# Optimization experiments

Measured on AMD Instinct MI355X. Metric: run time of the kernel, lower is better.

The kernel has to match this reference:

```python
import jax, jax.numpy as jnp
import numpy as np

B, S, D, H = 4, 1024, 1024, 16
HD = D // H  # 64
EPS = 1e-5

def _ln(x, g, b):
    m = jnp.mean(x, axis=-1, keepdims=True)
    v = jnp.mean(jnp.square(x - m), axis=-1, keepdims=True)
    return (x - m) * jax.lax.rsqrt(v + EPS) * g + b

def setup_inputs() -> dict:
    key = jax.random.key(0)
    ks = jax.random.split(key, 16)
    std = 0.02
    return {
        "query_tokens": jax.random.normal(ks[0], (B, S, D), jnp.float32),
        "keyvalue_tokens": jax.random.normal(ks[1], (B, S, D), jnp.float32),
        "ln_q_g": jnp.ones((D,), jnp.float32),
        "ln_q_b": jnp.zeros((D,), jnp.float32),
        "ln_kv_g": jnp.ones((D,), jnp.float32),
        "ln_kv_b": jnp.zeros((D,), jnp.float32),
        "Wq": jax.random.normal(ks[2], (2 * D, D), jnp.float32) * std,
        "Wk": jax.random.normal(ks[3], (2 * D, D), jnp.float32) * std,
        "Wv": jax.random.normal(ks[4], (2 * D, D), jnp.float32) * std,
        "Wo": jax.random.normal(ks[5], (D, 2 * D), jnp.float32) * std,
        "lambda_q1": jax.random.normal(ks[6], (HD,), jnp.float32) * 0.1,
        "lambda_k1": jax.random.normal(ks[7], (HD,), jnp.float32) * 0.1,
        "lambda_q2": jax.random.normal(ks[8], (HD,), jnp.float32) * 0.1,
        "lambda_k2": jax.random.normal(ks[9], (HD,), jnp.float32) * 0.1,
        "hn_g": jnp.ones((2 * HD,), jnp.float32),
        "hn_b": jnp.zeros((2 * HD,), jnp.float32),
        "lambda_init": jnp.float32(0.8),
        "disable_second_term": 0,
    }

def reference(query_tokens, keyvalue_tokens, ln_q_g, ln_q_b, ln_kv_g, ln_kv_b,
              Wq, Wk, Wv, Wo, lambda_q1, lambda_k1, lambda_q2, lambda_k2,
              hn_g, hn_b, lambda_init, disable_second_term):
    scale = 1.0 / np.sqrt(HD)
    q_ln = _ln(query_tokens, ln_q_g, ln_q_b)
    kv_ln = _ln(keyvalue_tokens, ln_kv_g, ln_kv_b)
    # projections: torch Linear => x @ W.T ; reshape to [B, H, S, 2*HD]
    def proj(x, W):
        y = jnp.einsum('bsd,ed->bse', x, W)
        return y.reshape(B, S, H, 2 * HD).transpose(0, 2, 1, 3)
    q = proj(q_ln, Wq)
    k = proj(kv_ln, Wk)
    v = proj(kv_ln, Wv)
    q1, q2 = q[..., :HD], q[..., HD:]
    k1, k2 = k[..., :HD], k[..., HD:]
    scores1 = jnp.einsum('bhsd,bhtd->bhst', q1, k1) * scale
    scores2 = jnp.einsum('bhsd,bhtd->bhst', q2, k2) * scale
    attn1 = jax.nn.softmax(scores1, axis=-1)
    attn2 = jax.nn.softmax(scores2, axis=-1)
    if disable_second_term:
        lam = jnp.zeros((), query_tokens.dtype)
    else:
        lam = (jnp.exp(jnp.dot(lambda_q1, lambda_k1))
               - jnp.exp(jnp.dot(lambda_q2, lambda_k2)) + lambda_init)
    out = jnp.einsum('bhst,bhtd->bhsd', attn1 - lam * attn2, v)  # [B,H,S,2HD]
    out = _ln(out, hn_g, hn_b) * (1.0 - lambda_init)
    out = out.transpose(0, 2, 1, 3).reshape(B, S, 2 * D)
    out = jnp.einsum('bse,de->bsd', out, Wo)
    return query_tokens + out
```

## Files before the change

kernel.cpp:

```cpp
#include <hip/hip_runtime.h>
#include <stdint.h>

#define B_  4
#define S_  1024
#define D_  1024
#define H_  16
#define HD_ 64
#define E_  2048
#define C2_ 128

typedef __attribute__((ext_vector_type(8))) short          bf16x8;
typedef __attribute__((ext_vector_type(8))) unsigned short u16x8;
typedef __attribute__((ext_vector_type(4))) unsigned short u16x4;
typedef __attribute__((ext_vector_type(4))) float          f32x4;

#define QSCALE 0.18033688f

__device__ __forceinline__ unsigned short f2bf(float f) {
  union { float f; unsigned int u; } v; v.f = f;
  unsigned int r = v.u + 0x7fffu + ((v.u >> 16) & 1u);
  return (unsigned short)(r >> 16);
}

__device__ __forceinline__ unsigned int cvtpk_bf16(float lo, float hi) {
  unsigned int r;
  asm("v_cvt_pk_bf16_f32 %0, %1, %2" : "=v"(r) : "v"(lo), "v"(hi));
  return r;
}

__device__ __forceinline__ float red16_sum(float x) {
  x += __int_as_float(__builtin_amdgcn_mov_dpp(__float_as_int(x), 0xB1, 0xF, 0xF, false));
  x += __int_as_float(__builtin_amdgcn_mov_dpp(__float_as_int(x), 0x4E, 0xF, 0xF, false));
  x += __int_as_float(__builtin_amdgcn_mov_dpp(__float_as_int(x), 0x141, 0xF, 0xF, false));
  x += __int_as_float(__builtin_amdgcn_mov_dpp(__float_as_int(x), 0x140, 0xF, 0xF, false));
  return x;
}

typedef const __attribute__((address_space(1))) unsigned int* gas1_t;
typedef __attribute__((address_space(3))) unsigned int* las3_t;
__device__ __forceinline__ void gload16(const void* g, void* s) {
  __builtin_amdgcn_global_load_lds((gas1_t)g, (las3_t)s, 16, 0, 0);
}

__global__ __launch_bounds__(256) void ln2_cast_k(const float* __restrict__ xq,
                                                  const float* __restrict__ xkv,
                                                  const float* __restrict__ gq,
                                                  const float* __restrict__ bq,
                                                  const float* __restrict__ gkv,
                                                  const float* __restrict__ bkv,
                                                  unsigned short* __restrict__ oq,
                                                  unsigned short* __restrict__ okv) {
  int sel = blockIdx.y;
  const float* x = sel ? xkv : xq;
  const float* g = sel ? gkv : gq;
  const float* bb = sel ? bkv : bq;
  unsigned short* out = sel ? okv : oq;
  int row = blockIdx.x;
  int tid = threadIdx.x;
  const float* xr = x + (size_t)row * D_;
  float4 xv = *(const float4*)(xr + tid * 4);
  float s  = xv.x + xv.y + xv.z + xv.w;
  float sq = xv.x * xv.x + xv.y * xv.y + xv.z * xv.z + xv.w * xv.w;
#pragma unroll
  for (int m = 32; m; m >>= 1) { s += __shfl_xor(s, m, 64); sq += __shfl_xor(sq, m, 64); }
  __shared__ float ps[4], pq[4];
  int w = tid >> 6, l = tid & 63;
  if (l == 0) { ps[w] = s; pq[w] = sq; }
  __syncthreads();
  s  = ps[0] + ps[1] + ps[2] + ps[3];
  sq = pq[0] + pq[1] + pq[2] + pq[3];
  float mean = s * (1.f / D_);
  float var  = sq * (1.f / D_) - mean * mean;
  float rstd = rsqrtf(var + 1e-5f);
  float4 gv = *(const float4*)(g + tid * 4);
  float4 bv = *(const float4*)(bb + tid * 4);
  u16x4 o;
  o.x = f2bf((xv.x - mean) * rstd * gv.x + bv.x);
  o.y = f2bf((xv.y - mean) * rstd * gv.y + bv.y);
  o.z = f2bf((xv.z - mean) * rstd * gv.z + bv.z);
  o.w = f2bf((xv.w - mean) * rstd * gv.w + bv.w);
  *(u16x4*)(out + (size_t)row * D_ + tid * 4) = o;
}

__global__ __launch_bounds__(256) void cast4_k(const float* __restrict__ i0, const float* __restrict__ i1,
                                               const float* __restrict__ i2, const float* __restrict__ i3,
                                               unsigned short* __restrict__ o0, unsigned short* __restrict__ o1,
                                               unsigned short* __restrict__ o2, unsigned short* __restrict__ o3,
                                               int n4) {
  int sel = blockIdx.y;
  const float* in = (sel == 0) ? i0 : (sel == 1) ? i1 : (sel == 2) ? i2 : i3;
  unsigned short* out = (sel == 0) ? o0 : (sel == 1) ? o1 : (sel == 2) ? o2 : o3;
  int i = blockIdx.x * 256 + threadIdx.x;
  if (i < n4) {
    float4 v = *(const float4*)(in + (size_t)i * 4);
    u16x4 o; o.x = f2bf(v.x); o.y = f2bf(v.y); o.z = f2bf(v.z); o.w = f2bf(v.w);
    *(u16x4*)(out + (size_t)i * 4) = o;
  }
}

__global__ __launch_bounds__(256) void gemm_proj_k(
    const unsigned short* __restrict__ qln, const unsigned short* __restrict__ kvln,
    const unsigned short* __restrict__ Wq,  const unsigned short* __restrict__ Wk,
    const unsigned short* __restrict__ Wv,
    unsigned short* __restrict__ qb, unsigned short* __restrict__ kb,
    unsigned short* __restrict__ vtb) {
  const int K = D_;
  int which = blockIdx.z;
  const unsigned short* A = (which == 0) ? qln : kvln;
  const unsigned short* W = (which == 0) ? Wq : (which == 1 ? Wk : Wv);
  unsigned short* O = (which == 0) ? qb : (which == 1 ? kb : vtb);
  int m0 = blockIdx.y * 128, n0 = blockIdx.x * 128;
  __shared__ __align__(16) char psm[128 * 272];
  char* lsA = psm;
  char* lsB = psm + 16384;
  int tid = threadIdx.x, l = tid & 63, w = tid >> 6;
  int wm = (w >> 1) * 64, wn = (w & 1) * 64;
  f32x4 acc[4][4] = {};
  for (int kt = 0; kt < K; kt += 64) {
    __syncthreads();
#pragma unroll
    for (int i = 0; i < 4; i++) {
      int rbase = (i * 4 + w) * 8;
      int row = rbase + (l >> 3), c8 = l & 7;
      int sc = (c8 ^ (row & 7)) * 8;
      gload16(A + (size_t)(m0 + row) * K + kt + sc, lsA + rbase * 128);
      gload16(W + (size_t)(n0 + row) * K + kt + sc, lsB + rbase * 128);
    }
    __syncthreads();
#pragma unroll
    for (int kk = 0; kk < 2; kk++) {
      bf16x8 af[4], bfr[4];
      int koff = kk * 64 + (l >> 4) * 16;
#pragma unroll
      for (int mf = 0; mf < 4; mf++) {
        int row = wm + mf * 16 + (l & 15);
        af[mf] = *(const bf16x8*)(lsA + row * 128 + (koff ^ ((row & 7) << 4)));
      }
#pragma unroll
      for (int nf = 0; nf < 4; nf++) {
        int row = wn + nf * 16 + (l & 15);
        bfr[nf] = *(const bf16x8*)(lsB + row * 128 + (koff ^ ((row & 7) << 4)));
      }
#pragma unroll
      for (int mf = 0; mf < 4; mf++)
#pragma unroll
        for (int nf = 0; nf < 4; nf++)
          acc[mf][nf] = __builtin_amdgcn_mfma_f32_16x16x32_bf16(af[mf], bfr[nf], acc[mf][nf], 0, 0, 0);
    }
  }
  if (which < 2) {
    float sc = (which == 0) ? QSCALE : 1.0f;
#pragma unroll
    for (int mf = 0; mf < 4; mf++)
#pragma unroll
      for (int nf = 0; nf < 4; nf++)
#pragma unroll
        for (int r = 0; r < 4; r++) {
          int gm = m0 + wm + mf * 16 + (l >> 4) * 4 + r;
          int gn = n0 + wn + nf * 16 + (l & 15);
          int b = gm >> 10, s = gm & 1023;
          int h = gn >> 7,  c = gn & 127;
          O[((size_t)((b * H_ + h) * S_ + s)) * C2_ + c] = f2bf(acc[mf][nf][r] * sc);
        }
  } else {
    __syncthreads();
#pragma unroll
    for (int mf = 0; mf < 4; mf++)
#pragma unroll
      for (int nf = 0; nf < 4; nf++) {
        int crow = wn + nf * 16 + (l & 15);
        int sloc = wm + mf * 16 + (l >> 4) * 4;
        u16x4 pk4;
        pk4.x = f2bf(acc[mf][nf][0]); pk4.y = f2bf(acc[mf][nf][1]);
        pk4.z = f2bf(acc[mf][nf][2]); pk4.w = f2bf(acc[mf][nf][3]);
        *(u16x4*)(psm + (size_t)crow * 272 + sloc * 2) = pk4;
      }
    __syncthreads();
    int b = m0 >> 10, sbase = m0 & 1023;
#pragma unroll
    for (int i = 0; i < 8; i++) {
      int u2 = i * 256 + tid;
      int row = u2 >> 4, c16 = u2 & 15;
      u16x8 vv = *(const u16x8*)(psm + (size_t)row * 272 + c16 * 16);
      int gn = n0 + row, h = gn >> 7, cfeat = gn & 127;
      *(u16x8*)(O + ((size_t)((b * H_ + h) * C2_ + cfeat)) * S_ + sbase + c16 * 8) = vv;
    }
  }
}

__global__ __launch_bounds__(256) void gemm_out_k(
    const unsigned short* __restrict__ A, const unsigned short* __restrict__ W,
    const float* __restrict__ resid, float* __restrict__ out) {
  const int K = E_;
  int m0 = blockIdx.y * 128, n0 = blockIdx.x * 128;
  __shared__ __align__(16) char psm2[32768];
  char* lsA = psm2;
  char* lsB = psm2 + 16384;
  int tid = threadIdx.x, l = tid & 63, w = tid >> 6;
  int wm = (w >> 1) * 64, wn = (w & 1) * 64;
  f32x4 acc[4][4] = {};
  for (int kt = 0; kt < K; kt += 64) {
    __syncthreads();
#pragma unroll
    for (int i = 0; i < 4; i++) {
      int rbase = (i * 4 + w) * 8;
      int row = rbase + (l >> 3), c8 = l & 7;
      int sc = (c8 ^ (row & 7)) * 8;
      gload16(A + (size_t)(m0 + row) * K + kt + sc, lsA + rbase * 128);
      gload16(W + (size_t)(n0 + row) * K + kt + sc, lsB + rbase * 128);
    }
    __syncthreads();
#pragma unroll
    for (int kk = 0; kk < 2; kk++) {
      bf16x8 af[4], bfr[4];
      int koff = kk * 64 + (l >> 4) * 16;
#pragma unroll
      for (int mf = 0; mf < 4; mf++) {
        int row = wm + mf * 16 + (l & 15);
        af[mf] = *(const bf16x8*)(lsA + row * 128 + (koff ^ ((row & 7) << 4)));
      }
#pragma unroll
      for (int nf = 0; nf < 4; nf++) {
        int row = wn + nf * 16 + (l & 15);
        bfr[nf] = *(const bf16x8*)(lsB + row * 128 + (koff ^ ((row & 7) << 4)));
      }
#pragma unroll
      for (int mf = 0; mf < 4; mf++)
#pragma unroll
        for (int nf = 0; nf < 4; nf++)
          acc[mf][nf] = __builtin_amdgcn_mfma_f32_16x16x32_bf16(af[mf], bfr[nf], acc[mf][nf], 0, 0, 0);
    }
  }
#pragma unroll
  for (int mf = 0; mf < 4; mf++)
#pragma unroll
    for (int nf = 0; nf < 4; nf++)
#pragma unroll
      for (int r = 0; r < 4; r++) {
        int gm = m0 + wm + mf * 16 + (l >> 4) * 4 + r;
        int gn = n0 + wn + nf * 16 + (l & 15);
        size_t idx = (size_t)gm * D_ + gn;
        out[idx] = acc[mf][nf][r] + resid[idx];
      }
}

__global__ __launch_bounds__(256) void attn_k(
    const unsigned short* __restrict__ q, const unsigned short* __restrict__ k,
    const unsigned short* __restrict__ vt,
    const float* __restrict__ lq1, const float* __restrict__ lk1,
    const float* __restrict__ lq2, const float* __restrict__ lk2,
    const float* __restrict__ hng, const float* __restrict__ hnb,
    const float* __restrict__ lambda_init, const int* __restrict__ dis2,
    unsigned short* __restrict__ out) {
  int bh = blockIdx.x;
  int qt = blockIdx.y;
  int tid = threadIdx.x, ln = tid & 63, w = tid >> 6;
  int g = ln >> 4, c = ln & 15;
  __shared__ unsigned short lsK[64 * 128];
  __shared__ unsigned short lsVt[128 * 64];
  __shared__ float s_lam, s_osc;

  if (tid < 64) {
    float a = lq1[ln] * lk1[ln];
    float cc = lq2[ln] * lk2[ln];
#pragma unroll
    for (int m = 32; m; m >>= 1) { a += __shfl_xor(a, m, 64); cc += __shfl_xor(cc, m, 64); }
    if (ln == 0) {
      float li = lambda_init[0];
      float lam = __expf(a) - __expf(cc) + li;
      if (dis2[0] != 0) lam = 0.f;
      s_lam = lam;
      s_osc = 1.f - li;
    }
  }

  const unsigned short* kbh = k + (size_t)bh * S_ * C2_;
  const unsigned short* vbh = vt + (size_t)bh * C2_ * S_;

  int qrow = qt * 64 + w * 16 + c;
  const unsigned short* qrp = q + ((size_t)bh * S_ + qrow) * C2_;
  bf16x8 qf[2][2];
#pragma unroll
  for (int t = 0; t < 2; t++)
#pragma unroll
    for (int kk = 0; kk < 2; kk++)
      qf[t][kk] = *(const bf16x8*)(qrp + t * 64 + kk * 32 + g * 8);

  f32x4 lones[2] = {};
  f32x4 o[2][8] = {};
  bf16x8 onesf;
#pragma unroll
  for (int j = 0; j < 8; j++) onesf[j] = (short)0x3F80;

#define STAGE_KV(t0s)                                                                 \
  {                                                                                   \
    const unsigned short* kbase = kbh + (size_t)(t0s) * C2_;                          \
    _Pragma("unroll")                                                                 \
    for (int i = 0; i < 4; i++) {                                                     \
      int rb = w * 16 + i * 4;                                                        \
      int row = rb + (ln >> 4), c16 = ln & 15;                                        \
      gload16(kbase + row * C2_ + ((c16 ^ (row & 7)) * 8),                            \
              (char*)&lsK[0] + rb * 256);                                             \
    }                                                                                 \
    const unsigned short* vbase = vbh + (t0s);                                        \
    _Pragma("unroll")                                                                 \
    for (int i = 0; i < 4; i++) {                                                     \
      int rb = w * 32 + i * 8;                                                        \
      int row = rb + (ln >> 3), c8 = ln & 7;                                          \
      gload16(vbase + (size_t)row * S_ + ((c8 ^ (row & 7)) * 8),                      \
              (char*)&lsVt[0] + rb * 128);                                            \
    }                                                                                 \
  }

  for (int t0 = 0; t0 < S_; t0 += 64) {
    STAGE_KV(t0);
    __syncthreads();

    unsigned int paw[2][2][4];

#pragma unroll
    for (int term = 0; term < 2; term++) {
      f32x4 sf[4] = {};
      __builtin_amdgcn_s_setprio(1);
#pragma unroll
      for (int kk = 0; kk < 2; kk++) {
#pragma unroll
        for (int nf = 0; nf < 4; nf++) {
          int kfrow = nf * 16 + c;
          bf16x8 kf = *(const bf16x8*)((char*)&lsK[0] + kfrow * 256 +
                        ((term * 128 + kk * 64 + g * 16) ^ ((kfrow & 7) << 4)));
          sf[nf] = __builtin_amdgcn_mfma_f32_16x16x32_bf16(kf, qf[term][kk], sf[nf], 0, 0, 0);
        }
      }
      __builtin_amdgcn_s_setprio(0);
#pragma unroll
      for (int nf = 0; nf < 4; nf++)
#pragma unroll
        for (int r = 0; r < 4; r++)
          sf[nf][r] = exp2f(sf[nf][r]);
#pragma unroll
      for (int kk = 0; kk < 2; kk++) {
        unsigned int X0 = cvtpk_bf16(sf[2 * kk][0], sf[2 * kk][1]);
        unsigned int X1 = cvtpk_bf16(sf[2 * kk][2], sf[2 * kk][3]);
        unsigned int Y0 = cvtpk_bf16(sf[2 * kk + 1][0], sf[2 * kk + 1][1]);
        unsigned int Y1 = cvtpk_bf16(sf[2 * kk + 1][2], sf[2 * kk + 1][3]);
        asm("v_permlane32_swap_b32 %0, %1" : "+v"(X0), "+v"(Y0));
        asm("v_permlane32_swap_b32 %0, %1" : "+v"(X1), "+v"(Y1));
        asm("v_permlane16_swap_b32 %0, %1" : "+v"(X0), "+v"(Y0));
        asm("v_permlane16_swap_b32 %0, %1" : "+v"(X1), "+v"(Y1));
        paw[term][kk][0] = X0; paw[term][kk][1] = X1;
        paw[term][kk][2] = Y0; paw[term][kk][3] = Y1;
      }
    }

#pragma unroll
    for (int kk = 0; kk < 2; kk++) {
      union { unsigned int u[4]; bf16x8 v; } pa0, pa1;
#pragma unroll
      for (int j = 0; j < 4; j++) { pa0.u[j] = paw[0][kk][j]; pa1.u[j] = paw[1][kk][j]; }
      __builtin_amdgcn_s_setprio(1);
      lones[0] = __builtin_amdgcn_mfma_f32_16x16x32_bf16(pa0.v, onesf, lones[0], 0, 0, 0);
      lones[1] = __builtin_amdgcn_mfma_f32_16x16x32_bf16(pa1.v, onesf, lones[1], 0, 0, 0);
#pragma unroll
      for (int nf2 = 0; nf2 < 8; nf2++) {
        int vrow = nf2 * 16 + c;
        bf16x8 vf = *(const bf16x8*)((char*)&lsVt[0] + vrow * 128 +
                      ((kk * 64 + g * 16) ^ ((vrow & 7) << 4)));
        o[0][nf2] = __builtin_amdgcn_mfma_f32_16x16x32_bf16(pa0.v, vf, o[0][nf2], 0, 0, 0);
        o[1][nf2] = __builtin_amdgcn_mfma_f32_16x16x32_bf16(pa1.v, vf, o[1][nf2], 0, 0, 0);
      }
      __builtin_amdgcn_s_setprio(0);
    }
    __syncthreads();
  }

  float lam = s_lam, osc = s_osc;
  int b = bh >> 4, h = bh & 15;
#pragma unroll
  for (int r = 0; r < 4; r++) {
    float inv1 = 1.f / lones[0][r];
    float inv2 = lam / lones[1][r];
    float vals[8];
    float sum = 0.f, sq = 0.f;
#pragma unroll
    for (int nf2 = 0; nf2 < 8; nf2++) {
      float vv = o[0][nf2][r] * inv1 - o[1][nf2][r] * inv2;
      vals[nf2] = vv;
      sum += vv; sq += vv * vv;
    }
    sum = red16_sum(sum);
    sq  = red16_sum(sq);
    float mean = sum * (1.f / 128.f);
    float var  = sq * (1.f / 128.f) - mean * mean;
    float rstd = rsqrtf(var + 1e-5f);
    int srow = qt * 64 + w * 16 + g * 4 + r;
    unsigned short* orow = out + ((size_t)(b * S_ + srow)) * E_ + h * C2_;
#pragma unroll
    for (int nf2 = 0; nf2 < 8; nf2++) {
      int feat = nf2 * 16 + c;
      float y = (vals[nf2] - mean) * rstd * hng[feat] + hnb[feat];
      orow[feat] = f2bf(y * osc);
    }
  }
}

extern "C" void kernel_launch(void* const* d_in, const int* in_sizes, int n_in,
                              void* d_out, int out_size, void* d_ws, size_t ws_size,
                              hipStream_t stream) {
  const float* qtok = (const float*)d_in[0];
  const float* kvtok = (const float*)d_in[1];
  const float* lnqg = (const float*)d_in[2];
  const float* lnqb = (const float*)d_in[3];
  const float* lnkg = (const float*)d_in[4];
  const float* lnkb = (const float*)d_in[5];
  const float* Wq = (const float*)d_in[6];
  const float* Wk = (const float*)d_in[7];
  const float* Wv = (const float*)d_in[8];
  const float* Wo = (const float*)d_in[9];
  const float* lq1 = (const float*)d_in[10];
  const float* lk1 = (const float*)d_in[11];
  const float* lq2 = (const float*)d_in[12];
  const float* lk2 = (const float*)d_in[13];
  const float* hng = (const float*)d_in[14];
  const float* hnb = (const float*)d_in[15];
  const float* lami = (const float*)d_in[16];
  const int*   dis2 = (const int*)d_in[17];
  float* outp = (float*)d_out;

  char* ws = (char*)d_ws;
  const size_t MB = 1024 * 1024;
  unsigned short* qln    = (unsigned short*)(ws + 0);
  unsigned short* kvln   = (unsigned short*)(ws + 8 * MB);
  unsigned short* attn_o = (unsigned short*)(ws + 0);
  unsigned short* Wqb = (unsigned short*)(ws + 16 * MB);
  unsigned short* Wkb = (unsigned short*)(ws + 20 * MB);
  unsigned short* Wvb = (unsigned short*)(ws + 24 * MB);
  unsigned short* Wob = (unsigned short*)(ws + 28 * MB);
  unsigned short* qb  = (unsigned short*)(ws + 32 * MB);
  unsigned short* kb  = (unsigned short*)(ws + 48 * MB);
  unsigned short* vtb = (unsigned short*)(ws + 64 * MB);

  ln2_cast_k<<<dim3(4096, 2), dim3(256), 0, stream>>>(qtok, kvtok, lnqg, lnqb, lnkg, lnkb, qln, kvln);
  cast4_k<<<dim3(2048, 4), dim3(256), 0, stream>>>(Wq, Wk, Wv, Wo, Wqb, Wkb, Wvb, Wob, 512 * 1024);
  gemm_proj_k<<<dim3(16, 32, 3), dim3(256), 0, stream>>>(qln, kvln, Wqb, Wkb, Wvb, qb, kb, vtb);
  attn_k<<<dim3(64, 16), dim3(256), 0, stream>>>(qb, kb, vtb, lq1, lk1, lq2, lk2,
                                                 hng, hnb, lami, dis2, attn_o);
  gemm_out_k<<<dim3(8, 32), dim3(256), 0, stream>>>(attn_o, Wob, qtok, outp);
}
```

Before: 206.3 us.

## Double-buffer K/V LDS tiles with 32-key chunks to overlap loads with MFMA

Splits the key loop into 32-key chunks and adds two LDS buffers for K and Vt, so the next chunk is prefetched while the current one is computed. The Vt LDS layout and swizzle change to fit the narrower tile. The goal is to hide global-to-LDS latency behind the matrix work. In exchange there are twice as many iterations and barriers, and each barrier covers less MFMA work.

```diff
diff --git a/kernel.cpp b/kernel.cpp
--- a/kernel.cpp
+++ b/kernel.cpp
@@ -256,8 +256,8 @@
   int qt = blockIdx.y;
   int tid = threadIdx.x, ln = tid & 63, w = tid >> 6;
   int g = ln >> 4, c = ln & 15;
-  __shared__ unsigned short lsK[64 * 128];
-  __shared__ unsigned short lsVt[128 * 64];
+  __shared__ unsigned short lsK[2][32 * 128];
+  __shared__ unsigned short lsVt[2][128 * 32];
   __shared__ float s_lam, s_osc;
 
   if (tid < 64) {
@@ -292,80 +292,81 @@
 #pragma unroll
   for (int j = 0; j < 8; j++) onesf[j] = (short)0x3F80;
 
-#define STAGE_KV(t0s)                                                                 \
+#define STAGE_KV(buf, t0s)                                                            \
   {                                                                                   \
     const unsigned short* kbase = kbh + (size_t)(t0s) * C2_;                          \
     _Pragma("unroll")                                                                 \
-    for (int i = 0; i < 4; i++) {                                                     \
-      int rb = w * 16 + i * 4;                                                        \
+    for (int i = 0; i < 2; i++) {                                                     \
+      int rb = w * 8 + i * 4;                                                         \
       int row = rb + (ln >> 4), c16 = ln & 15;                                        \
       gload16(kbase + row * C2_ + ((c16 ^ (row & 7)) * 8),                            \
-              (char*)&lsK[0] + rb * 256);                                             \
+              (char*)&lsK[buf][0] + rb * 256);                                        \
     }                                                                                 \
     const unsigned short* vbase = vbh + (t0s);                                        \
     _Pragma("unroll")                                                                 \
-    for (int i = 0; i < 4; i++) {                                                     \
-      int rb = w * 32 + i * 8;                                                        \
-      int row = rb + (ln >> 3), c8 = ln & 7;                                          \
-      gload16(vbase + (size_t)row * S_ + ((c8 ^ (row & 7)) * 8),                      \
-              (char*)&lsVt[0] + rb * 128);                                            \
+    for (int i = 0; i < 2; i++) {                                                     \
+      int rb = w * 32 + i * 16;                                                       \
+      int row = rb + (ln >> 2), c4 = ln & 3;                                          \
+      gload16(vbase + (size_t)row * S_ + ((c4 ^ ((row >> 1) & 3)) * 8),               \
+              (char*)&lsVt[buf][0] + rb * 64);                                        \
     }                                                                                 \
   }
 
-  for (int t0 = 0; t0 < S_; t0 += 64) {
-    STAGE_KV(t0);
-    __syncthreads();
-
-    unsigned int paw[2][2][4];
+  STAGE_KV(0, 0);
+  __syncthreads();
+
+  for (int it = 0; it < S_ / 32; ++it) {
+    int cur = it & 1;
+    if (it + 1 < S_ / 32) STAGE_KV(cur ^ 1, (it + 1) * 32);
+
+    unsigned int paw[2][4];
 
 #pragma unroll
     for (int term = 0; term < 2; term++) {
-      f32x4 sf[4] = {};
+      f32x4 sf[2] = {};
       __builtin_amdgcn_s_setprio(1);
 #pragma unroll
       for (int kk = 0; kk < 2; kk++) {
 #pragma unroll
-        for (int nf = 0; nf < 4; nf++) {
+        for (int nf = 0; nf < 2; nf++) {
           int kfrow = nf * 16 + c;
-          bf16x8 kf = *(const bf16x8*)((char*)&lsK[0] + kfrow * 256 +
+          bf16x8 kf = *(const bf16x8*)((char*)&lsK[cur][0] + kfrow * 256 +
                         ((term * 128 + kk * 64 + g * 16) ^ ((kfrow & 7) << 4)));
           sf[nf] = __builtin_amdgcn_mfma_f32_16x16x32_bf16(kf, qf[term][kk], sf[nf], 0, 0, 0);
         }
       }
       __builtin_amdgcn_s_setprio(0);
 #pragma unroll
-      for (int nf = 0; nf < 4; nf++)
+      for (int nf = 0; nf < 2; nf++)
 #pragma unroll
         for (int r = 0; r < 4; r++)
           sf[nf][r] = exp2f(sf[nf][r]);
-#pragma unroll
-      for (int kk = 0; kk < 2; kk++) {
-        unsigned int X0 = cvtpk_bf16(sf[2 * kk][0], sf[2 * kk][1]);
-        unsigned int X1 = cvtpk_bf16(sf[2 * kk][2], sf[2 * kk][3]);
-        unsigned int Y0 = cvtpk_bf16(sf[2 * kk + 1][0], sf[2 * kk + 1][1]);
-        unsigned int Y1 = cvtpk_bf16(sf[2 * kk + 1][2], sf[2 * kk + 1][3]);
+      {
+        unsigned int X0 = cvtpk_bf16(sf[0][0], sf[0][1]);
+        unsigned int X1 = cvtpk_bf16(sf[0][2], sf[0][3]);
+        unsigned int Y0 = cvtpk_bf16(sf[1][0], sf[1][1]);
+        unsigned int Y1 = cvtpk_bf16(sf[1][2], sf[1][3]);
         asm("v_permlane32_swap_b32 %0, %1" : "+v"(X0), "+v"(Y0));
         asm("v_permlane32_swap_b32 %0, %1" : "+v"(X1), "+v"(Y1));
         asm("v_permlane16_swap_b32 %0, %1" : "+v"(X0), "+v"(Y0));
         asm("v_permlane16_swap_b32 %0, %1" : "+v"(X1), "+v"(Y1));
-        paw[term][kk][0] = X0; paw[term][kk][1] = X1;
-        paw[term][kk][2] = Y0; paw[term][kk][3] = Y1;
-      }
-    }
-
-#pragma unroll
-    for (int kk = 0; kk < 2; kk++) {
+        paw[term][0] = X0; paw[term][1] = X1;
+        paw[term][2] = Y0; paw[term][3] = Y1;
+      }
+    }
+
+    {
       union { unsigned int u[4]; bf16x8 v; } pa0, pa1;
 #pragma unroll
-      for (int j = 0; j < 4; j++) { pa0.u[j] = paw[0][kk][j]; pa1.u[j] = paw[1][kk][j]; }
+      for (int j = 0; j < 4; j++) { pa0.u[j] = paw[0][j]; pa1.u[j] = paw[1][j]; }
       __builtin_amdgcn_s_setprio(1);
       lones[0] = __builtin_amdgcn_mfma_f32_16x16x32_bf16(pa0.v, onesf, lones[0], 0, 0, 0);
       lones[1] = __builtin_amdgcn_mfma_f32_16x16x32_bf16(pa1.v, onesf, lones[1], 0, 0, 0);
 #pragma unroll
       for (int nf2 = 0; nf2 < 8; nf2++) {
         int vrow = nf2 * 16 + c;
-        bf16x8 vf = *(const bf16x8*)((char*)&lsVt[0] + vrow * 128 +
-                      ((kk * 64 + g * 16) ^ ((vrow & 7) << 4)));
+        bf16x8 vf = *(const bf16x8*)((char*)&lsVt[cur][0] + vrow * 64 +
+                      ((g * 16) ^ (((vrow >> 1) & 3) << 4)));
         o[0][nf2] = __builtin_amdgcn_mfma_f32_16x16x32_bf16(pa0.v, vf, o[0][nf2], 0, 0, 0);
         o[1][nf2] = __builtin_amdgcn_mfma_f32_16x16x32_bf16(pa1.v, vf, o[1][nf2], 0, 0, 0);
       }
```

Result: slower. 218.9 us (+6.1%).

## Prefetch next K/V tiles during attention compute and merge prep kernels

Applied to the files above, without the earlier changes.

The attention loop now issues the next K tile's global-to-LDS DMA after score computation and loads the next V tile into registers early, writing it to LDS after the PV MFMAs. This overlaps memory latency with compute instead of stalling at the top of each iteration. The layer-norm cast and weight cast kernels are also merged into one launch with extra grid rows, which removes one launch. The attention loop gains one extra barrier per iteration and uses more registers, which may lower occupancy. Weight-cast blocks beyond 2048 exit early.

```diff
diff --git a/kernel.cpp b/kernel.cpp
--- a/kernel.cpp
+++ b/kernel.cpp
@@ -42,21 +42,36 @@
   __builtin_amdgcn_global_load_lds((gas1_t)g, (las3_t)s, 16, 0, 0);
 }
 
-__global__ __launch_bounds__(256) void ln2_cast_k(const float* __restrict__ xq,
-                                                  const float* __restrict__ xkv,
-                                                  const float* __restrict__ gq,
-                                                  const float* __restrict__ bq,
-                                                  const float* __restrict__ gkv,
-                                                  const float* __restrict__ bkv,
-                                                  unsigned short* __restrict__ oq,
-                                                  unsigned short* __restrict__ okv) {
-  int sel = blockIdx.y;
-  const float* x = sel ? xkv : xq;
-  const float* g = sel ? gkv : gq;
-  const float* bb = sel ? bkv : bq;
-  unsigned short* out = sel ? okv : oq;
+__global__ __launch_bounds__(256) void pre_k(const float* __restrict__ xq,
+                                             const float* __restrict__ xkv,
+                                             const float* __restrict__ gq,
+                                             const float* __restrict__ bq,
+                                             const float* __restrict__ gkv,
+                                             const float* __restrict__ bkv,
+                                             unsigned short* __restrict__ oq,
+                                             unsigned short* __restrict__ okv,
+                                             const float* __restrict__ w0, const float* __restrict__ w1,
+                                             const float* __restrict__ w2, const float* __restrict__ w3,
+                                             unsigned short* __restrict__ wo0, unsigned short* __restrict__ wo1,
+                                             unsigned short* __restrict__ wo2, unsigned short* __restrict__ wo3) {
+  int y = blockIdx.y;
+  int tid = threadIdx.x;
+  if (y >= 2) {
+    int i = blockIdx.x * 256 + tid;
+    if (i >= 512 * 1024) return;
+    int sel = y - 2;
+    const float* in = (sel == 0) ? w0 : (sel == 1) ? w1 : (sel == 2) ? w2 : w3;
+    unsigned short* out = (sel == 0) ? wo0 : (sel == 1) ? wo1 : (sel == 2) ? wo2 : wo3;
+    float4 v = *(const float4*)(in + (size_t)i * 4);
+    u16x4 o; o.x = f2bf(v.x); o.y = f2bf(v.y); o.z = f2bf(v.z); o.w = f2bf(v.w);
+    *(u16x4*)(out + (size_t)i * 4) = o;
+    return;
+  }
+  const float* x = y ? xkv : xq;
+  const float* g = y ? gkv : gq;
+  const float* bb = y ? bkv : bq;
+  unsigned short* out = y ? okv : oq;
   int row = blockIdx.x;
-  int tid = threadIdx.x;
   const float* xr = x + (size_t)row * D_;
   float4 xv = *(const float4*)(xr + tid * 4);
   float s  = xv.x + xv.y + xv.z + xv.w;
@@ -80,22 +95,6 @@
   o.z = f2bf((xv.z - mean) * rstd * gv.z + bv.z);
   o.w = f2bf((xv.w - mean) * rstd * gv.w + bv.w);
   *(u16x4*)(out + (size_t)row * D_ + tid * 4) = o;
-}
-
-__global__ __launch_bounds__(256) void cast4_k(const float* __restrict__ i0, const float* __restrict__ i1,
-                                               const float* __restrict__ i2, const float* __restrict__ i3,
-                                               unsigned short* __restrict__ o0, unsigned short* __restrict__ o1,
-                                               unsigned short* __restrict__ o2, unsigned short* __restrict__ o3,
-                                               int n4) {
-  int sel = blockIdx.y;
-  const float* in = (sel == 0) ? i0 : (sel == 1) ? i1 : (sel == 2) ? i2 : i3;
-  unsigned short* out = (sel == 0) ? o0 : (sel == 1) ? o1 : (sel == 2) ? o2 : o3;
-  int i = blockIdx.x * 256 + threadIdx.x;
-  if (i < n4) {
-    float4 v = *(const float4*)(in + (size_t)i * 4);
-    u16x4 o; o.x = f2bf(v.x); o.y = f2bf(v.y); o.z = f2bf(v.z); o.w = f2bf(v.w);
-    *(u16x4*)(out + (size_t)i * 4) = o;
-  }
 }
 
 __global__ __launch_bounds__(256) void gemm_proj_k(
@@ -292,7 +291,10 @@
 #pragma unroll
   for (int j = 0; j < 8; j++) onesf[j] = (short)0x3F80;
 
-#define STAGE_KV(t0s)                                                                 \
+  int vc8 = ln & 7;
+  int vrow0 = w * 32 + (ln >> 3);
+
+#define STAGE_K(t0s)                                                                  \
   {                                                                                   \
     const unsigned short* kbase = kbh + (size_t)(t0s) * C2_;                          \
     _Pragma("unroll")                                                                 \
@@ -302,6 +304,9 @@
       gload16(kbase + row * C2_ + ((c16 ^ (row & 7)) * 8),                            \
               (char*)&lsK[0] + rb * 256);                                             \
     }                                                                                 \
+  }
+#define STAGE_V_DMA(t0s)                                                              \
+  {                                                                                   \
     const unsigned short* vbase = vbh + (t0s);                                        \
     _Pragma("unroll")                                                                 \
     for (int i = 0; i < 4; i++) {                                                     \
@@ -312,9 +317,22 @@
     }                                                                                 \
   }
 
-  for (int t0 = 0; t0 < S_; t0 += 64) {
-    STAGE_KV(t0);
-    __syncthreads();
+  STAGE_K(0);
+  STAGE_V_DMA(0);
+  __syncthreads();
+
+  for (int it = 0; it < S_ / 64; ++it) {
+    bool havenext = (it + 1 < S_ / 64);
+    int t0n = (it + 1) * 64;
+
+    u16x8 vr0, vr1, vr2, vr3;
+    if (havenext) {
+      const unsigned short* vbase = vbh + t0n;
+      vr0 = *(const u16x8*)(vbase + (size_t)(vrow0 +  0) * S_ + vc8 * 8);
+      vr1 = *(const u16x8*)(vbase + (size_t)(vrow0 +  8) * S_ + vc8 * 8);
+      vr2 = *(const u16x8*)(vbase + (size_t)(vrow0 + 16) * S_ + vc8 * 8);
+      vr3 = *(const u16x8*)(vbase + (size_t)(vrow0 + 24) * S_ + vc8 * 8);
+    }
 
     unsigned int paw[2][2][4];
 
@@ -353,6 +371,9 @@
       }
     }
 
+    __syncthreads();
+    if (havenext) STAGE_K(t0n);
+
 #pragma unroll
     for (int kk = 0; kk < 2; kk++) {
       union { unsigned int u[4]; bf16x8 v; } pa0, pa1;
@@ -370,6 +391,14 @@
         o[1][nf2] = __builtin_amdgcn_mfma_f32_16x16x32_bf16(pa1.v, vf, o[1][nf2], 0, 0, 0);
       }
       __builtin_amdgcn_s_setprio(0);
+    }
+
+    __syncthreads();
+    if (havenext) {
+      *(u16x8*)((char*)&lsVt[0] + (vrow0 +  0) * 128 + ((vc8 ^ ((vrow0 +  0) & 7)) * 16)) = vr0;
+      *(u16x8*)((char*)&lsVt[0] + (vrow0 +  8) * 128 + ((vc8 ^ ((vrow0 +  8) & 7)) * 16)) = vr1;
+      *(u16x8*)((char*)&lsVt[0] + (vrow0 + 16) * 128 + ((vc8 ^ ((vrow0 + 16) & 7)) * 16)) = vr2;
+      *(u16x8*)((char*)&lsVt[0] + (vrow0 + 24) * 128 + ((vc8 ^ ((vrow0 + 24) & 7)) * 16)) = vr3;
     }
     __syncthreads();
   }
@@ -440,8 +469,8 @@
   unsigned short* kb  = (unsigned short*)(ws + 48 * MB);
   unsigned short* vtb = (unsigned short*)(ws + 64 * MB);
 
-  ln2_cast_k<<<dim3(4096, 2), dim3(256), 0, stream>>>(qtok, kvtok, lnqg, lnqb, lnkg, lnkb, qln, kvln);
-  cast4_k<<<dim3(2048, 4), dim3(256), 0, stream>>>(Wq, Wk, Wv, Wo, Wqb, Wkb, Wvb, Wob, 512 * 1024);
+  pre_k<<<dim3(4096, 6), dim3(256), 0, stream>>>(qtok, kvtok, lnqg, lnqb, lnkg, lnkb, qln, kvln,
+                                                 Wq, Wk, Wv, Wo, Wqb, Wkb, Wvb, Wob);
   gemm_proj_k<<<dim3(16, 32, 3), dim3(256), 0, stream>>>(qln, kvln, Wqb, Wkb, Wvb, qb, kb, vtb);
   attn_k<<<dim3(64, 16), dim3(256), 0, stream>>>(qb, kb, vtb, lq1, lk1, lq2, lk2,
                                                  hng, hnb, lami, dis2, attn_o);
```

After: 204.7 us. Within noise of the previous version (-0.7%).
